# Kernel optimization log

Measured on AMD Instinct MI355X. Metric: run time of the kernel, lower is better.

The kernel has to match this reference:

```python
import jax, jax.numpy as jnp
import numpy as np

BIT = 8
QMAX = 2 ** (BIT - 1) - 1   # 127
QMIN = -(2 ** (BIT - 1))    # -128


def _quant_linear(x, W, b, act_sf):
    """HAWQ-style QuantLinear: per-output-channel symmetric 8-bit weights,
    integer GEMM on the (already-quantized) activation grid, dequantized output.
    Returns (out, weight_scaling_factor)."""
    w_sf = jnp.max(jnp.abs(W), axis=1) / QMAX                      # [out]
    w_int = jnp.clip(jnp.round(W / w_sf[:, None]), QMIN, QMAX)     # [out,in]
    x_int = x / act_sf                                             # integer-valued floats
    b_int = jnp.round(b / (w_sf * act_sf))                         # [out]
    out = (jnp.einsum('bsd,od->bso', x_int, w_int) + b_int) * (w_sf * act_sf)
    return out, w_sf


def _quant_act(x):
    """QuantAct: per-tensor symmetric 8-bit requantization."""
    sf = jnp.max(jnp.abs(x)) / QMAX
    xq = jnp.clip(jnp.round(x / sf), QMIN, QMAX) * sf
    return xq, sf


def setup_inputs() -> dict:
    key = jax.random.key(0)
    k = jax.random.split(key, 5)
    B, S, D, H = 256, 196, 384, 1536
    act_scaling_factor = jnp.array([0.05], jnp.float32)
    x = jax.random.normal(k[0], (B, S, D), jnp.float32)
    # input arrives already fake-quantized on the act_scaling_factor grid
    x = jnp.clip(jnp.round(x / act_scaling_factor), QMIN, QMAX) * act_scaling_factor
    W1 = jax.random.normal(k[1], (H, D), jnp.float32) * 0.02
    b1 = jax.random.normal(k[2], (H,), jnp.float32) * 0.02
    W2 = jax.random.normal(k[3], (D, H), jnp.float32) * 0.02
    b2 = jax.random.normal(k[4], (D,), jnp.float32) * 0.02
    return dict(x=x, W1=W1, b1=b1, W2=W2, b2=b2,
                act_scaling_factor=act_scaling_factor)


def reference(x, W1, b1, W2, b2, act_scaling_factor):
    h, _ = _quant_linear(x, W1, b1, act_scaling_factor)
    h = jax.nn.relu(h)
    h, asf1 = _quant_act(h)
    y, _ = _quant_linear(h, W2, b2, asf1)
    y, asf2 = _quant_act(y)
    return y, asf2
```

## Files before the change

kernel.cpp:

```cpp
#include <hip/hip_runtime.h>
#include <hip/hip_bf16.h>
#include <stdint.h>


#define M_TOT 50176
#define D_IN  384
#define H_MID 1536
#define OUT_N (M_TOT * D_IN)
#define NSLOT 256

typedef int v4i __attribute__((ext_vector_type(4)));

__device__ __forceinline__ float clamp_q(float q) {
  return fminf(fmaxf(q, -128.0f), 127.0f);
}

__device__ __forceinline__ float fast_div(float t, float d, float R) {
  const float q1 = t * R;
  const float r  = fmaf(-d, q1, t);
  return fmaf(r, R, q1);
}

__device__ __forceinline__ void gld_lds16(const int8_t* g, int8_t* s) {
  __builtin_amdgcn_global_load_lds((const __attribute__((address_space(1))) void*)g,
                                   (__attribute__((address_space(3))) void*)s,
                                   16, 0, 0);
}


__global__ void quant_w_kernel(const float* __restrict__ W, const float* __restrict__ b,
                               int8_t* __restrict__ Wq, float* __restrict__ wsf,
                               int* __restrict__ bint, const float* __restrict__ asf_p,
                               int cols) {
  const int lane = threadIdx.x & 63;
  const int row  = blockIdx.x * 4 + (threadIdx.x >> 6);
  const float* wr = W + (size_t)row * cols;
  float m = 0.f;
  for (int c = lane; c < cols; c += 64) m = fmaxf(m, fabsf(wr[c]));
#pragma unroll
  for (int off = 32; off; off >>= 1) m = fmaxf(m, __shfl_xor(m, off));
  const float sf = m / 127.0f;
  int8_t* qbase = Wq + (size_t)(row >> 4) * 16 * cols + (row & 15) * 16;
  for (int c = lane; c < cols; c += 64)
    qbase[(c >> 4) * 256 + (c & 15)] = (int8_t)clamp_q(rintf(wr[c] / sf));
  if (lane == 0) {
    wsf[row] = sf;
    if (bint) bint[row] = (int)rintf(b[row] / (sf * asf_p[0]));
  }
}

__global__ void quant_x_kernel(const float* __restrict__ x, int8_t* __restrict__ xq,
                               const float* __restrict__ asf_p) {
  const int lane = threadIdx.x & 63;
  const int wid  = threadIdx.x >> 6;
  const float R = 1.0f / asf_p[0];
  const int r  = lane & 15;
  const int kq = lane >> 4;
  const int ntask = (M_TOT / 16) * 6;
  for (int task = blockIdx.x * 4 + wid; task < ntask; task += gridDim.x * 4) {
    const int pan = task / 6;
    const int kcq = task - pan * 6;
    const float* src = x + ((size_t)pan * 16 + r) * D_IN + (kcq * 4 + kq) * 16;
    int out[4];
#pragma unroll
    for (int q4 = 0; q4 < 4; ++q4) {
      float4 v = *(const float4*)(src + q4 * 4);
      unsigned a0 = (unsigned char)(signed char)clamp_q(rintf(v.x * R));
      unsigned a1 = (unsigned char)(signed char)clamp_q(rintf(v.y * R));
      unsigned a2 = (unsigned char)(signed char)clamp_q(rintf(v.z * R));
      unsigned a3 = (unsigned char)(signed char)clamp_q(rintf(v.w * R));
      out[q4] = (int)(a0 | (a1 << 8) | (a2 << 16) | (a3 << 24));
    }
    *(int4*)(xq + (size_t)pan * 6144 + kcq * 1024 + lane * 16) = *(int4*)out;
  }
}

template <int MODE>
__global__ __launch_bounds__(512, 4) void gemm1_i8_kernel(
    const int8_t* __restrict__ A, const int8_t* __restrict__ Bm,
    const float* __restrict__ sfv, const int* __restrict__ bintv,
    const float* __restrict__ asf_p, const unsigned* __restrict__ gmax_in,
    int8_t* __restrict__ Cq, unsigned* __restrict__ gmax_out) {
  const int K = D_IN;
  __shared__ __align__(16) int8_t sA[2][8192];
  __shared__ __align__(16) int8_t sB[2][16384];
  const int tid    = threadIdx.x;
  const int lane   = tid & 63;
  const int wid    = tid >> 6;
  const int wr     = wid >> 2;
  const int wc     = wid & 3;
  const int tid16  = tid * 16;
  const int lane16 = lane * 16;
  const int l16    = lane & 15;
  const int r0     = (lane >> 4) * 4;
  const int cpx = gridDim.x >> 3;
  const int wg  = (blockIdx.x & 7) * cpx + (blockIdx.x >> 3);
  const int bm = wg % (H_MID / 128);
  const int bn = wg / (H_MID / 128);

  const int8_t* gA0 = A  + (size_t)(bm * 8)  * (16 * K);
  const int8_t* gB0 = Bm + (size_t)(bn * 16) * (16 * K);
  const int fA = tid16;
  const int baseA = (fA >> 10) * 16 * K + (fA & 1023);
  int baseB[2];
#pragma unroll
  for (int l = 0; l < 2; ++l) {
    const int f = l * 8192 + tid16;
    baseB[l] = (f >> 10) * 16 * K + (f & 1023);
  }

  v4i acc[4][4] = {};
  const int niter = K >> 6;

  gld_lds16(gA0 + baseA, &sA[0][tid16]);
#pragma unroll
  for (int l = 0; l < 2; ++l) gld_lds16(gB0 + baseB[l], &sB[0][l * 8192 + tid16]);

  for (int c = 0; c < niter; ++c) {
    const int buf = c & 1;
    if (c + 1 < niter) {
      const int co = (c + 1) << 10;
      gld_lds16(gA0 + baseA + co, &sA[buf ^ 1][tid16]);
#pragma unroll
      for (int l = 0; l < 2; ++l)
        gld_lds16(gB0 + baseB[l] + co, &sB[buf ^ 1][l * 8192 + tid16]);
      asm volatile("s_waitcnt vmcnt(3)" ::: "memory");
    } else {
      asm volatile("s_waitcnt vmcnt(0)" ::: "memory");
    }
    __builtin_amdgcn_s_barrier();
    __builtin_amdgcn_sched_barrier(0);
    v4i af[4], bf[4];
#pragma unroll
    for (int i = 0; i < 4; ++i)
      af[i] = *(const v4i*)&sA[buf][(wr * 4 + i) * 1024 + lane16];
#pragma unroll
    for (int j = 0; j < 4; ++j)
      bf[j] = *(const v4i*)&sB[buf][(wc * 4 + j) * 1024 + lane16];
#pragma unroll
    for (int i = 0; i < 4; ++i)
#pragma unroll
      for (int j = 0; j < 4; ++j)
        acc[i][j] = __builtin_amdgcn_mfma_i32_16x16x64_i8(af[i], bf[j], acc[i][j], 0, 0, 0);
    __builtin_amdgcn_sched_barrier(0);
    __builtin_amdgcn_s_barrier();
  }

  float lmax = 0.f;
  if (MODE == 0) {
    const float asf = asf_p[0];
#pragma unroll
    for (int i = 0; i < 4; ++i) {
      const int hbase = bm * 128 + wr * 64 + i * 16 + r0;
#pragma unroll
      for (int r = 0; r < 4; ++r) {
        int mi = acc[i][0][r];
#pragma unroll
        for (int j = 1; j < 4; ++j) mi = max(mi, acc[i][j][r]);
        const int h = hbase + r;
        lmax = fmaxf(lmax, (float)(mi + bintv[h]) * (sfv[h] * asf));
      }
    }
#pragma unroll
    for (int off = 32; off; off >>= 1) lmax = fmaxf(lmax, __shfl_xor(lmax, off));
    if (lane == 0) atomicMax(&gmax_out[(wg * 8 + wid) & (NSLOT - 1)], __float_as_uint(lmax));
  } else {
    float m = fmaxf(fmaxf(__uint_as_float(gmax_in[lane]),
                          __uint_as_float(gmax_in[lane + 64])),
                    fmaxf(__uint_as_float(gmax_in[lane + 128]),
                          __uint_as_float(gmax_in[lane + 192])));
#pragma unroll
    for (int off = 32; off; off >>= 1) m = fmaxf(m, __shfl_xor(m, off));
    const float sf1 = m / 127.0f;
    const float asf = asf_p[0];
    const float R   = 1.0f / sf1;
#pragma unroll
    for (int i = 0; i < 4; ++i) {
      const int hbase = bm * 128 + wr * 64 + i * 16 + r0;
      const int htile = bm * 8 + wr * 4 + i;
      float ratio[4];
      int bi4[4];
#pragma unroll
      for (int r = 0; r < 4; ++r) {
        const int h = hbase + r;
        ratio[r] = fast_div(sfv[h] * asf, sf1, R);
        bi4[r]   = bintv[h];
      }
#pragma unroll
      for (int j = 0; j < 4; ++j) {
        const int mm = bn * 256 + wc * 64 + j * 16 + l16;
        unsigned d = 0;
#pragma unroll
        for (int r = 0; r < 4; ++r) {
          const float f = (float)(acc[i][j][r] + bi4[r]);
          const int q = (int)fminf(fmaxf(rintf(f * ratio[r]), 0.f), 127.f);
          d |= (unsigned)q << (8 * r);
        }
        *(unsigned*)(Cq + (size_t)(mm >> 4) * 24576 + htile * 256 + (mm & 15) * 16 + r0) = d;
      }
    }
  }
}

__global__ __launch_bounds__(256, 4) void gemm2_i8_kernel(
    const int8_t* __restrict__ A, const int8_t* __restrict__ Bm,
    const float* __restrict__ sfv, const float* __restrict__ bias,
    const unsigned* __restrict__ gmax_in,
    float* __restrict__ Cout, unsigned* __restrict__ gmax_out) {
  const int K = H_MID;
  __shared__ __align__(16) int8_t sA[2][8192];
  __shared__ __align__(16) int8_t sB[2][8192];
  const int tid    = threadIdx.x;
  const int lane   = tid & 63;
  const int wid    = tid >> 6;
  const int wr     = wid >> 1;
  const int wc     = wid & 1;
  const int tid16  = tid * 16;
  const int lane16 = lane * 16;
  const int l16    = lane & 15;
  const int r0     = (lane >> 4) * 4;
  const int cpx = gridDim.x >> 3;
  const int wg  = (blockIdx.x & 7) * cpx + (blockIdx.x >> 3);
  const int bm = wg / (D_IN / 128);
  const int bn = wg % (D_IN / 128);

  const int8_t* gA0 = A  + (size_t)(bm * 8) * (16 * K);
  const int8_t* gB0 = Bm + (size_t)(bn * 8) * (16 * K);
  int base[2];
#pragma unroll
  for (int l = 0; l < 2; ++l) {
    const int f = l * 4096 + tid16;
    base[l] = (f >> 10) * 16 * K + (f & 1023);
  }

  v4i acc[4][4] = {};
  const int niter = K >> 6;

#pragma unroll
  for (int l = 0; l < 2; ++l) gld_lds16(gA0 + base[l], &sA[0][l * 4096 + tid16]);
#pragma unroll
  for (int l = 0; l < 2; ++l) gld_lds16(gB0 + base[l], &sB[0][l * 4096 + tid16]);

  for (int c = 0; c < niter; ++c) {
    const int buf = c & 1;
    if (c + 1 < niter) {
      const int co = (c + 1) << 10;
#pragma unroll
      for (int l = 0; l < 2; ++l)
        gld_lds16(gA0 + base[l] + co, &sA[buf ^ 1][l * 4096 + tid16]);
#pragma unroll
      for (int l = 0; l < 2; ++l)
        gld_lds16(gB0 + base[l] + co, &sB[buf ^ 1][l * 4096 + tid16]);
      asm volatile("s_waitcnt vmcnt(4)" ::: "memory");
    } else {
      asm volatile("s_waitcnt vmcnt(0)" ::: "memory");
    }
    __builtin_amdgcn_s_barrier();
    __builtin_amdgcn_sched_barrier(0);
    v4i af[4], bf[4];
#pragma unroll
    for (int i = 0; i < 4; ++i)
      af[i] = *(const v4i*)&sA[buf][(wr * 4 + i) * 1024 + lane16];
#pragma unroll
    for (int j = 0; j < 4; ++j)
      bf[j] = *(const v4i*)&sB[buf][(wc * 4 + j) * 1024 + lane16];
#pragma unroll
    for (int i = 0; i < 4; ++i)
#pragma unroll
      for (int j = 0; j < 4; ++j)
        acc[i][j] = __builtin_amdgcn_mfma_i32_16x16x64_i8(af[i], bf[j], acc[i][j], 0, 0, 0);
    __builtin_amdgcn_sched_barrier(0);
    __builtin_amdgcn_s_barrier();
  }

  float m = fmaxf(fmaxf(__uint_as_float(gmax_in[lane]),
                        __uint_as_float(gmax_in[lane + 64])),
                  fmaxf(__uint_as_float(gmax_in[lane + 128]),
                        __uint_as_float(gmax_in[lane + 192])));
#pragma unroll
  for (int off = 32; off; off >>= 1) m = fmaxf(m, __shfl_xor(m, off));
  const float sf1 = m / 127.0f;

  float lmax = 0.f;
#pragma unroll
  for (int j = 0; j < 4; ++j) {
    const int d = bn * 128 + wc * 64 + j * 16 + l16;
    const float scale = sfv[d] * sf1;
    const int bi = (int)rintf(bias[d] / scale);
    int mi = acc[0][j][0], mn = acc[0][j][0];
#pragma unroll
    for (int i = 0; i < 4; ++i) {
      const int row = bm * 128 + wr * 64 + i * 16 + r0;
#pragma unroll
      for (int r = 0; r < 4; ++r) {
        const int a = acc[i][j][r];
        mi = max(mi, a); mn = min(mn, a);
        Cout[(size_t)(row + r) * D_IN + d] = (float)(a + bi) * scale;
      }
    }
    lmax = fmaxf(lmax, fmaxf(fabsf((float)(mi + bi) * scale),
                             fabsf((float)(mn + bi) * scale)));
  }
#pragma unroll
  for (int off = 32; off; off >>= 1) lmax = fmaxf(lmax, __shfl_xor(lmax, off));
  if (lane == 0) atomicMax(&gmax_out[(wg * 4 + wid) & (NSLOT - 1)], __float_as_uint(lmax));
}

__global__ void final_quant_kernel(float* __restrict__ y, const unsigned* __restrict__ slots,
                                   int n4) {
  __shared__ float s_sf;
  const int tid = threadIdx.x;
  if (tid < 64) {
    float m = fmaxf(fmaxf(__uint_as_float(slots[tid]),
                          __uint_as_float(slots[tid + 64])),
                    fmaxf(__uint_as_float(slots[tid + 128]),
                          __uint_as_float(slots[tid + 192])));
#pragma unroll
    for (int off = 32; off; off >>= 1) m = fmaxf(m, __shfl_xor(m, off));
    if (tid == 0) s_sf = m / 127.0f;
  }
  __syncthreads();
  const float asf2 = s_sf;
  const float R = 1.0f / asf2;
  float4* y4 = (float4*)y;
  const int stride = gridDim.x * blockDim.x;
  for (int i = blockIdx.x * blockDim.x + tid; i < n4; i += stride) {
    float4 v = y4[i];
    v.x = clamp_q(rintf(fast_div(v.x, asf2, R))) * asf2;
    v.y = clamp_q(rintf(fast_div(v.y, asf2, R))) * asf2;
    v.z = clamp_q(rintf(fast_div(v.z, asf2, R))) * asf2;
    v.w = clamp_q(rintf(fast_div(v.w, asf2, R))) * asf2;
    y4[i] = v;
  }
  if (blockIdx.x == 0 && tid == 0) y[(size_t)n4 * 4] = asf2;
}

extern "C" void kernel_launch(void* const* d_in, const int* in_sizes, int n_in,
                              void* d_out, int out_size, void* d_ws, size_t ws_size,
                              hipStream_t stream) {
  const float* x   = (const float*)d_in[0];
  const float* W1  = (const float*)d_in[1];
  const float* b1  = (const float*)d_in[2];
  const float* W2  = (const float*)d_in[3];
  const float* b2  = (const float*)d_in[4];
  const float* asf = (const float*)d_in[5];

  char* ws = (char*)d_ws;
  unsigned* gmax1 = (unsigned*)ws;
  unsigned* gmax2 = (unsigned*)(ws + 1024);
  size_t off = 4096;
  int8_t* xq   = (int8_t*)(ws + off); off += (size_t)M_TOT * D_IN;
  int8_t* w1q  = (int8_t*)(ws + off); off += (size_t)H_MID * D_IN;
  float*  w1sf = (float*)(ws + off);  off += (size_t)H_MID * 4;
  int*    b1i  = (int*)(ws + off);    off += (size_t)H_MID * 4;
  int8_t* w2q  = (int8_t*)(ws + off); off += (size_t)D_IN * H_MID;
  float*  w2sf = (float*)(ws + off);  off += (size_t)D_IN * 4;
  off = (off + 255) & ~(size_t)255;
  int8_t* hq   = (int8_t*)(ws + off); off += (size_t)M_TOT * H_MID;

  hipMemsetAsync(d_ws, 0, 4096, stream);

  quant_w_kernel<<<H_MID / 4, 256, 0, stream>>>(W1, b1, w1q, w1sf, b1i, asf, D_IN);
  quant_w_kernel<<<D_IN / 4, 256, 0, stream>>>(W2, nullptr, w2q, w2sf, nullptr, nullptr, H_MID);
  quant_x_kernel<<<2048, 256, 0, stream>>>(x, xq, asf);

  const int g1 = (H_MID / 128) * (M_TOT / 256);
  const int g2 = (M_TOT / 128) * (D_IN / 128);
  gemm1_i8_kernel<0><<<g1, 512, 0, stream>>>(
      w1q, xq, w1sf, b1i, asf, nullptr, nullptr, gmax1);
  gemm1_i8_kernel<1><<<g1, 512, 0, stream>>>(
      w1q, xq, w1sf, b1i, asf, gmax1, hq, nullptr);
  gemm2_i8_kernel<<<g2, 256, 0, stream>>>(
      hq, w2q, w2sf, b2, gmax1, (float*)d_out, gmax2);
  final_quant_kernel<<<2048, 256, 0, stream>>>((float*)d_out, gmax2, OUT_N / 4);
}
```

Baseline: 196.6 us.

## Load weight fragments directly into registers, stage only activations in LDS

Both int8 GEMMs now read the weight operand straight from global memory into per-wave register double buffers instead of staging it through LDS, so only the activation tile uses shared memory. GEMM1 shrinks from 512-thread 128x256 tiles to 256-thread 128x128 tiles, doubling its grid, and the K loop is unrolled by two to alternate the register buffers. This is meant to cut LDS traffic and footprint and raise occupancy. In exchange, waves that share a weight panel each load it separately from global memory, and the smaller GEMM1 tiles reuse each weight load across fewer activation rows.

Result: slower. 228.0 us (+16.0%).

```diff
diff --git a/kernel.cpp b/kernel.cpp
--- a/kernel.cpp
+++ b/kernel.cpp
@@ -76,19 +76,18 @@
 }
 
 template <int MODE>
-__global__ __launch_bounds__(512, 4) void gemm1_i8_kernel(
-    const int8_t* __restrict__ A, const int8_t* __restrict__ Bm,
+__global__ __launch_bounds__(256, 4) void gemm1_i8_kernel(
+    const int8_t* __restrict__ Wq, const int8_t* __restrict__ Xq,
     const float* __restrict__ sfv, const int* __restrict__ bintv,
     const float* __restrict__ asf_p, const unsigned* __restrict__ gmax_in,
     int8_t* __restrict__ Cq, unsigned* __restrict__ gmax_out) {
   const int K = D_IN;
-  __shared__ __align__(16) int8_t sA[2][8192];
-  __shared__ __align__(16) int8_t sB[2][16384];
+  __shared__ __align__(16) int8_t sV[2][8192];
   const int tid    = threadIdx.x;
   const int lane   = tid & 63;
   const int wid    = tid >> 6;
-  const int wr     = wid >> 2;
-  const int wc     = wid & 3;
+  const int wr     = wid >> 1;
+  const int wc     = wid & 1;
   const int tid16  = tid * 16;
   const int lane16 = lane * 16;
   const int l16    = lane & 15;
@@ -98,53 +97,59 @@
   const int bm = wg % (H_MID / 128);
   const int bn = wg / (H_MID / 128);
 
-  const int8_t* gA0 = A  + (size_t)(bm * 8)  * (16 * K);
-  const int8_t* gB0 = Bm + (size_t)(bn * 16) * (16 * K);
-  const int fA = tid16;
-  const int baseA = (fA >> 10) * 16 * K + (fA & 1023);
-  int baseB[2];
+  const int sK = 16 * K;
+  const int8_t* pa = Wq + (size_t)(bm * 8 + wr * 4) * sK + lane16;
+  const int8_t* gV = Xq + (size_t)(bn * 8) * sK;
+  int baseV[2];
 #pragma unroll
   for (int l = 0; l < 2; ++l) {
-    const int f = l * 8192 + tid16;
-    baseB[l] = (f >> 10) * 16 * K + (f & 1023);
+    const int f = l * 4096 + tid16;
+    baseV[l] = (f >> 10) * sK + (f & 1023);
   }
 
   v4i acc[4][4] = {};
+  v4i d0[4], d1[4];
   const int niter = K >> 6;
 
-  gld_lds16(gA0 + baseA, &sA[0][tid16]);
-#pragma unroll
-  for (int l = 0; l < 2; ++l) gld_lds16(gB0 + baseB[l], &sB[0][l * 8192 + tid16]);
-
-  for (int c = 0; c < niter; ++c) {
-    const int buf = c & 1;
-    if (c + 1 < niter) {
-      const int co = (c + 1) << 10;
-      gld_lds16(gA0 + baseA + co, &sA[buf ^ 1][tid16]);
-#pragma unroll
-      for (int l = 0; l < 2; ++l)
-        gld_lds16(gB0 + baseB[l] + co, &sB[buf ^ 1][l * 8192 + tid16]);
-      asm volatile("s_waitcnt vmcnt(3)" ::: "memory");
-    } else {
-      asm volatile("s_waitcnt vmcnt(0)" ::: "memory");
-    }
-    __builtin_amdgcn_s_barrier();
-    __builtin_amdgcn_sched_barrier(0);
-    v4i af[4], bf[4];
-#pragma unroll
-    for (int i = 0; i < 4; ++i)
-      af[i] = *(const v4i*)&sA[buf][(wr * 4 + i) * 1024 + lane16];
-#pragma unroll
-    for (int j = 0; j < 4; ++j)
-      bf[j] = *(const v4i*)&sB[buf][(wc * 4 + j) * 1024 + lane16];
-#pragma unroll
-    for (int i = 0; i < 4; ++i)
-#pragma unroll
-      for (int j = 0; j < 4; ++j)
-        acc[i][j] = __builtin_amdgcn_mfma_i32_16x16x64_i8(af[i], bf[j], acc[i][j], 0, 0, 0);
-    __builtin_amdgcn_sched_barrier(0);
-    __builtin_amdgcn_s_barrier();
-  }
+#pragma unroll
+  for (int l = 0; l < 2; ++l) gld_lds16(gV + baseV[l], &sV[0][l * 4096 + tid16]);
+#pragma unroll
+  for (int i = 0; i < 4; ++i) d0[i] = *(const v4i*)(pa + i * sK);
+
+#define G1_BODY(c, buf, dc, dn)                                                   \
+  {                                                                               \
+    if ((c) + 1 < niter) {                                                        \
+      const int co = ((c) + 1) << 10;                                             \
+      _Pragma("unroll")                                                           \
+      for (int i = 0; i < 4; ++i) dn[i] = *(const v4i*)(pa + i * sK + co);        \
+      _Pragma("unroll")                                                           \
+      for (int l = 0; l < 2; ++l)                                                 \
+        gld_lds16(gV + baseV[l] + co, &sV[(buf) ^ 1][l * 4096 + tid16]);          \
+      asm volatile("s_waitcnt vmcnt(6)" ::: "memory");                            \
+    } else {                                                                      \
+      asm volatile("s_waitcnt vmcnt(0)" ::: "memory");                            \
+    }                                                                             \
+    __builtin_amdgcn_s_barrier();                                                 \
+    __builtin_amdgcn_sched_barrier(0);                                            \
+    v4i vf[4];                                                                    \
+    _Pragma("unroll")                                                             \
+    for (int j = 0; j < 4; ++j)                                                   \
+      vf[j] = *(const v4i*)&sV[(buf)][(wc * 4 + j) * 1024 + lane16];              \
+    _Pragma("unroll")                                                             \
+    for (int i = 0; i < 4; ++i)                                                   \
+      _Pragma("unroll")                                                           \
+      for (int j = 0; j < 4; ++j)                                                 \
+        acc[i][j] = __builtin_amdgcn_mfma_i32_16x16x64_i8(dc[i], vf[j],           \
+                                                          acc[i][j], 0, 0, 0);    \
+    __builtin_amdgcn_sched_barrier(0);                                            \
+    __builtin_amdgcn_s_barrier();                                                 \
+  }
+
+  for (int c = 0; c < niter; c += 2) {
+    G1_BODY(c,     0, d0, d1)
+    G1_BODY(c + 1, 1, d1, d0)
+  }
+#undef G1_BODY
 
   float lmax = 0.f;
   if (MODE == 0) {
@@ -163,7 +168,7 @@
     }
 #pragma unroll
     for (int off = 32; off; off >>= 1) lmax = fmaxf(lmax, __shfl_xor(lmax, off));
-    if (lane == 0) atomicMax(&gmax_out[(wg * 8 + wid) & (NSLOT - 1)], __float_as_uint(lmax));
+    if (lane == 0) atomicMax(&gmax_out[(wg * 4 + wid) & (NSLOT - 1)], __float_as_uint(lmax));
   } else {
     float m = fmaxf(fmaxf(__uint_as_float(gmax_in[lane]),
                           __uint_as_float(gmax_in[lane + 64])),
@@ -188,7 +193,7 @@
       }
 #pragma unroll
       for (int j = 0; j < 4; ++j) {
-        const int mm = bn * 256 + wc * 64 + j * 16 + l16;
+        const int mm = bn * 128 + wc * 64 + j * 16 + l16;
         unsigned d = 0;
 #pragma unroll
         for (int r = 0; r < 4; ++r) {
@@ -203,13 +208,12 @@
 }
 
 __global__ __launch_bounds__(256, 4) void gemm2_i8_kernel(
-    const int8_t* __restrict__ A, const int8_t* __restrict__ Bm,
+    const int8_t* __restrict__ Hq, const int8_t* __restrict__ W2q,
     const float* __restrict__ sfv, const float* __restrict__ bias,
     const unsigned* __restrict__ gmax_in,
     float* __restrict__ Cout, unsigned* __restrict__ gmax_out) {
   const int K = H_MID;
-  __shared__ __align__(16) int8_t sA[2][8192];
-  __shared__ __align__(16) int8_t sB[2][8192];
+  __shared__ __align__(16) int8_t sV[2][8192];
   const int tid    = threadIdx.x;
   const int lane   = tid & 63;
   const int wid    = tid >> 6;
@@ -224,54 +228,59 @@
   const int bm = wg / (D_IN / 128);
   const int bn = wg % (D_IN / 128);
 
-  const int8_t* gA0 = A  + (size_t)(bm * 8) * (16 * K);
-  const int8_t* gB0 = Bm + (size_t)(bn * 8) * (16 * K);
-  int base[2];
+  const int sK = 16 * K;
+  const int8_t* pb = W2q + (size_t)(bn * 8 + wc * 4) * sK + lane16;
+  const int8_t* gV = Hq + (size_t)(bm * 8) * sK;
+  int baseV[2];
 #pragma unroll
   for (int l = 0; l < 2; ++l) {
     const int f = l * 4096 + tid16;
-    base[l] = (f >> 10) * 16 * K + (f & 1023);
+    baseV[l] = (f >> 10) * sK + (f & 1023);
   }
 
   v4i acc[4][4] = {};
+  v4i d0[4], d1[4];
   const int niter = K >> 6;
 
 #pragma unroll
-  for (int l = 0; l < 2; ++l) gld_lds16(gA0 + base[l], &sA[0][l * 4096 + tid16]);
-#pragma unroll
-  for (int l = 0; l < 2; ++l) gld_lds16(gB0 + base[l], &sB[0][l * 4096 + tid16]);
-
-  for (int c = 0; c < niter; ++c) {
-    const int buf = c & 1;
-    if (c + 1 < niter) {
-      const int co = (c + 1) << 10;
-#pragma unroll
-      for (int l = 0; l < 2; ++l)
-        gld_lds16(gA0 + base[l] + co, &sA[buf ^ 1][l * 4096 + tid16]);
-#pragma unroll
-      for (int l = 0; l < 2; ++l)
-        gld_lds16(gB0 + base[l] + co, &sB[buf ^ 1][l * 4096 + tid16]);
-      asm volatile("s_waitcnt vmcnt(4)" ::: "memory");
-    } else {
-      asm volatile("s_waitcnt vmcnt(0)" ::: "memory");
-    }
-    __builtin_amdgcn_s_barrier();
-    __builtin_amdgcn_sched_barrier(0);
-    v4i af[4], bf[4];
-#pragma unroll
-    for (int i = 0; i < 4; ++i)
-      af[i] = *(const v4i*)&sA[buf][(wr * 4 + i) * 1024 + lane16];
-#pragma unroll
-    for (int j = 0; j < 4; ++j)
-      bf[j] = *(const v4i*)&sB[buf][(wc * 4 + j) * 1024 + lane16];
-#pragma unroll
-    for (int i = 0; i < 4; ++i)
-#pragma unroll
-      for (int j = 0; j < 4; ++j)
-        acc[i][j] = __builtin_amdgcn_mfma_i32_16x16x64_i8(af[i], bf[j], acc[i][j], 0, 0, 0);
-    __builtin_amdgcn_sched_barrier(0);
-    __builtin_amdgcn_s_barrier();
-  }
+  for (int l = 0; l < 2; ++l) gld_lds16(gV + baseV[l], &sV[0][l * 4096 + tid16]);
+#pragma unroll
+  for (int j = 0; j < 4; ++j) d0[j] = *(const v4i*)(pb + j * sK);
+
+#define G2_BODY(c, buf, dc, dn)                                                   \
+  {                                                                               \
+    if ((c) + 1 < niter) {                                                        \
+      const int co = ((c) + 1) << 10;                                             \
+      _Pragma("unroll")                                                           \
+      for (int j = 0; j < 4; ++j) dn[j] = *(const v4i*)(pb + j * sK + co);        \
+      _Pragma("unroll")                                                           \
+      for (int l = 0; l < 2; ++l)                                                 \
+        gld_lds16(gV + baseV[l] + co, &sV[(buf) ^ 1][l * 4096 + tid16]);          \
+      asm volatile("s_waitcnt vmcnt(6)" ::: "memory");                            \
+    } else {                                                                      \
+      asm volatile("s_waitcnt vmcnt(0)" ::: "memory");                            \
+    }                                                                             \
+    __builtin_amdgcn_s_barrier();                                                 \
+    __builtin_amdgcn_sched_barrier(0);                                            \
+    v4i af[4];                                                                    \
+    _Pragma("unroll")                                                             \
+    for (int i = 0; i < 4; ++i)                                                   \
+      af[i] = *(const v4i*)&sV[(buf)][(wr * 4 + i) * 1024 + lane16];              \
+    _Pragma("unroll")                                                             \
+    for (int i = 0; i < 4; ++i)                                                   \
+      _Pragma("unroll")                                                           \
+      for (int j = 0; j < 4; ++j)                                                 \
+        acc[i][j] = __builtin_amdgcn_mfma_i32_16x16x64_i8(af[i], dc[j],           \
+                                                          acc[i][j], 0, 0, 0);    \
+    __builtin_amdgcn_sched_barrier(0);                                            \
+    __builtin_amdgcn_s_barrier();                                                 \
+  }
+
+  for (int c = 0; c < niter; c += 2) {
+    G2_BODY(c,     0, d0, d1)
+    G2_BODY(c + 1, 1, d1, d0)
+  }
+#undef G2_BODY
 
   float m = fmaxf(fmaxf(__uint_as_float(gmax_in[lane]),
                         __uint_as_float(gmax_in[lane + 64])),
@@ -364,11 +373,11 @@
   quant_w_kernel<<<D_IN / 4, 256, 0, stream>>>(W2, nullptr, w2q, w2sf, nullptr, nullptr, H_MID);
   quant_x_kernel<<<2048, 256, 0, stream>>>(x, xq, asf);
 
-  const int g1 = (H_MID / 128) * (M_TOT / 256);
+  const int g1 = (H_MID / 128) * (M_TOT / 128);
   const int g2 = (M_TOT / 128) * (D_IN / 128);
-  gemm1_i8_kernel<0><<<g1, 512, 0, stream>>>(
+  gemm1_i8_kernel<0><<<g1, 256, 0, stream>>>(
       w1q, xq, w1sf, b1i, asf, nullptr, nullptr, gmax1);
-  gemm1_i8_kernel<1><<<g1, 512, 0, stream>>>(
+  gemm1_i8_kernel<1><<<g1, 256, 0, stream>>>(
       w1q, xq, w1sf, b1i, asf, gmax1, hq, nullptr);
   gemm2_i8_kernel<<<g2, 256, 0, stream>>>(
       hq, w2q, w2sf, b2, gmax1, (float*)d_out, gmax2);
```

## Switch int8 GEMMs to 32x32x32 MFMA with 32-row panel layout

Applied to the files above, without the earlier changes.

Replaces the 16x16x64 int8 MFMA tiles in both GEMM kernels with 32x32x32 MFMA instructions accumulating into 16-register outputs. The weight and activation quantization kernels now pack operands into 32-row panels so that each LDS fragment load feeds the larger instruction, and the epilogues are remapped to the 32x32 accumulator layout. The goal is fewer MFMA issues and fewer LDS fragment reads per unit of work, at the cost of a different output store pattern and reworked index math in every kernel.

After: 212.3 us. 8.0% more time.

```diff
diff --git a/kernel.cpp b/kernel.cpp
--- a/kernel.cpp
+++ b/kernel.cpp
@@ -9,7 +9,8 @@
 #define OUT_N (M_TOT * D_IN)
 #define NSLOT 256
 
-typedef int v4i __attribute__((ext_vector_type(4)));
+typedef int v4i  __attribute__((ext_vector_type(4)));
+typedef int v16i __attribute__((ext_vector_type(16)));
 
 __device__ __forceinline__ float clamp_q(float q) {
   return fminf(fmaxf(q, -128.0f), 127.0f);
@@ -26,7 +27,6 @@
                                    (__attribute__((address_space(3))) void*)s,
                                    16, 0, 0);
 }
-
 
 __global__ void quant_w_kernel(const float* __restrict__ W, const float* __restrict__ b,
                                int8_t* __restrict__ Wq, float* __restrict__ wsf,
@@ -40,9 +40,9 @@
 #pragma unroll
   for (int off = 32; off; off >>= 1) m = fmaxf(m, __shfl_xor(m, off));
   const float sf = m / 127.0f;
-  int8_t* qbase = Wq + (size_t)(row >> 4) * 16 * cols + (row & 15) * 16;
+  int8_t* qbase = Wq + (size_t)(row >> 5) * 32 * cols + (row & 31) * 16;
   for (int c = lane; c < cols; c += 64)
-    qbase[(c >> 4) * 256 + (c & 15)] = (int8_t)clamp_q(rintf(wr[c] / sf));
+    qbase[(c >> 4) * 512 + (c & 15)] = (int8_t)clamp_q(rintf(wr[c] / sf));
   if (lane == 0) {
     wsf[row] = sf;
     if (bint) bint[row] = (int)rintf(b[row] / (sf * asf_p[0]));
@@ -54,13 +54,13 @@
   const int lane = threadIdx.x & 63;
   const int wid  = threadIdx.x >> 6;
   const float R = 1.0f / asf_p[0];
-  const int r  = lane & 15;
-  const int kq = lane >> 4;
-  const int ntask = (M_TOT / 16) * 6;
+  const int r5 = lane & 31;
+  const int kh = lane >> 5;
+  const int ntask = (M_TOT / 32) * (D_IN / 32);
   for (int task = blockIdx.x * 4 + wid; task < ntask; task += gridDim.x * 4) {
-    const int pan = task / 6;
-    const int kcq = task - pan * 6;
-    const float* src = x + ((size_t)pan * 16 + r) * D_IN + (kcq * 4 + kq) * 16;
+    const int pan = task / 12;
+    const int t   = task - pan * 12;
+    const float* src = x + ((size_t)pan * 32 + r5) * D_IN + t * 32 + kh * 16;
     int out[4];
 #pragma unroll
     for (int q4 = 0; q4 < 4; ++q4) {
@@ -71,7 +71,7 @@
       unsigned a3 = (unsigned char)(signed char)clamp_q(rintf(v.w * R));
       out[q4] = (int)(a0 | (a1 << 8) | (a2 << 16) | (a3 << 24));
     }
-    *(int4*)(xq + (size_t)pan * 6144 + kcq * 1024 + lane * 16) = *(int4*)out;
+    *(int4*)(xq + (size_t)pan * (32 * D_IN) + t * 1024 + lane * 16) = *(int4*)out;
   }
 }
 
@@ -91,25 +91,24 @@
   const int wc     = wid & 3;
   const int tid16  = tid * 16;
   const int lane16 = lane * 16;
-  const int l16    = lane & 15;
-  const int r0     = (lane >> 4) * 4;
+  const int c5     = lane & 31;
+  const int hi     = lane >> 5;
   const int cpx = gridDim.x >> 3;
   const int wg  = (blockIdx.x & 7) * cpx + (blockIdx.x >> 3);
   const int bm = wg % (H_MID / 128);
   const int bn = wg / (H_MID / 128);
 
-  const int8_t* gA0 = A  + (size_t)(bm * 8)  * (16 * K);
-  const int8_t* gB0 = Bm + (size_t)(bn * 16) * (16 * K);
-  const int fA = tid16;
-  const int baseA = (fA >> 10) * 16 * K + (fA & 1023);
+  const int8_t* gA0 = A  + (size_t)(bm * 4) * (32 * K);
+  const int8_t* gB0 = Bm + (size_t)(bn * 8) * (32 * K);
+  const int baseA = (tid16 >> 11) * (32 * K) + (tid16 & 2047);
   int baseB[2];
 #pragma unroll
   for (int l = 0; l < 2; ++l) {
     const int f = l * 8192 + tid16;
-    baseB[l] = (f >> 10) * 16 * K + (f & 1023);
-  }
-
-  v4i acc[4][4] = {};
+    baseB[l] = (f >> 11) * (32 * K) + (f & 2047);
+  }
+
+  v16i acc[2][2] = {};
   const int niter = K >> 6;
 
   gld_lds16(gA0 + baseA, &sA[0][tid16]);
@@ -119,7 +118,7 @@
   for (int c = 0; c < niter; ++c) {
     const int buf = c & 1;
     if (c + 1 < niter) {
-      const int co = (c + 1) << 10;
+      const int co = (c + 1) << 11;
       gld_lds16(gA0 + baseA + co, &sA[buf ^ 1][tid16]);
 #pragma unroll
       for (int l = 0; l < 2; ++l)
@@ -130,18 +129,24 @@
     }
     __builtin_amdgcn_s_barrier();
     __builtin_amdgcn_sched_barrier(0);
-    v4i af[4], bf[4];
-#pragma unroll
-    for (int i = 0; i < 4; ++i)
-      af[i] = *(const v4i*)&sA[buf][(wr * 4 + i) * 1024 + lane16];
-#pragma unroll
-    for (int j = 0; j < 4; ++j)
-      bf[j] = *(const v4i*)&sB[buf][(wc * 4 + j) * 1024 + lane16];
-#pragma unroll
-    for (int i = 0; i < 4; ++i)
-#pragma unroll
-      for (int j = 0; j < 4; ++j)
-        acc[i][j] = __builtin_amdgcn_mfma_i32_16x16x64_i8(af[i], bf[j], acc[i][j], 0, 0, 0);
+    v4i af[2][2], bf[2][2];
+#pragma unroll
+    for (int ks = 0; ks < 2; ++ks) {
+#pragma unroll
+      for (int i = 0; i < 2; ++i)
+        af[ks][i] = *(const v4i*)&sA[buf][(wr * 2 + i) * 2048 + ks * 1024 + lane16];
+#pragma unroll
+      for (int j = 0; j < 2; ++j)
+        bf[ks][j] = *(const v4i*)&sB[buf][(wc * 2 + j) * 2048 + ks * 1024 + lane16];
+    }
+#pragma unroll
+    for (int ks = 0; ks < 2; ++ks)
+#pragma unroll
+      for (int i = 0; i < 2; ++i)
+#pragma unroll
+        for (int j = 0; j < 2; ++j)
+          acc[i][j] = __builtin_amdgcn_mfma_i32_32x32x32_i8(af[ks][i], bf[ks][j],
+                                                            acc[i][j], 0, 0, 0);
     __builtin_amdgcn_sched_barrier(0);
     __builtin_amdgcn_s_barrier();
   }
@@ -150,14 +155,12 @@
   if (MODE == 0) {
     const float asf = asf_p[0];
 #pragma unroll
-    for (int i = 0; i < 4; ++i) {
-      const int hbase = bm * 128 + wr * 64 + i * 16 + r0;
-#pragma unroll
-      for (int r = 0; r < 4; ++r) {
-        int mi = acc[i][0][r];
-#pragma unroll
-        for (int j = 1; j < 4; ++j) mi = max(mi, acc[i][j][r]);
-        const int h = hbase + r;
+    for (int i = 0; i < 2; ++i) {
+      const int hbase = bm * 128 + wr * 64 + i * 32;
+#pragma unroll
+      for (int reg = 0; reg < 16; ++reg) {
+        const int mi = max(acc[i][0][reg], acc[i][1][reg]);
+        const int h  = hbase + (reg & 3) + 8 * (reg >> 2) + 4 * hi;
         lmax = fmaxf(lmax, (float)(mi + bintv[h]) * (sfv[h] * asf));
       }
     }
@@ -175,35 +178,38 @@
     const float asf = asf_p[0];
     const float R   = 1.0f / sf1;
 #pragma unroll
-    for (int i = 0; i < 4; ++i) {
-      const int hbase = bm * 128 + wr * 64 + i * 16 + r0;
-      const int htile = bm * 8 + wr * 4 + i;
-      float ratio[4];
-      int bi4[4];
-#pragma unroll
-      for (int r = 0; r < 4; ++r) {
-        const int h = hbase + r;
-        ratio[r] = fast_div(sfv[h] * asf, sf1, R);
-        bi4[r]   = bintv[h];
+    for (int i = 0; i < 2; ++i) {
+#pragma unroll
+      for (int q = 0; q < 4; ++q) {
+        const int h0 = bm * 128 + wr * 64 + i * 32 + q * 8 + hi * 4;
+        float ratio[4];
+        int bi4[4];
+#pragma unroll
+        for (int r = 0; r < 4; ++r) {
+          const int h = h0 + r;
+          ratio[r] = fast_div(sfv[h] * asf, sf1, R);
+          bi4[r]   = bintv[h];
+        }
+#pragma unroll
+        for (int j = 0; j < 2; ++j) {
+          const int mm = bn * 256 + wc * 64 + j * 32 + c5;
+          unsigned d = 0;
+#pragma unroll
+          for (int r = 0; r < 4; ++r) {
+            const float f = (float)(acc[i][j][q * 4 + r] + bi4[r]);
+            const int qv = (int)fminf(fmaxf(rintf(f * ratio[r]), 0.f), 127.f);
+            d |= (unsigned)qv << (8 * r);
+          }
+          *(unsigned*)(Cq + (size_t)(mm >> 5) * 49152 + (h0 >> 4) * 512 +
+                       (mm & 31) * 16 + (h0 & 15)) = d;
+        }
       }
-#pragma unroll
-      for (int j = 0; j < 4; ++j) {
-        const int mm = bn * 256 + wc * 64 + j * 16 + l16;
-        unsigned d = 0;
-#pragma unroll
-        for (int r = 0; r < 4; ++r) {
-          const float f = (float)(acc[i][j][r] + bi4[r]);
-          const int q = (int)fminf(fmaxf(rintf(f * ratio[r]), 0.f), 127.f);
-          d |= (unsigned)q << (8 * r);
-        }
-        *(unsigned*)(Cq + (size_t)(mm >> 4) * 24576 + htile * 256 + (mm & 15) * 16 + r0) = d;
-      }
     }
   }
 }
 
 __global__ __launch_bounds__(256, 4) void gemm2_i8_kernel(
-    const int8_t* __restrict__ A, const int8_t* __restrict__ Bm,
+    const int8_t* __restrict__ Hq, const int8_t* __restrict__ W2q,
     const float* __restrict__ sfv, const float* __restrict__ bias,
     const unsigned* __restrict__ gmax_in,
     float* __restrict__ Cout, unsigned* __restrict__ gmax_out) {
@@ -217,23 +223,23 @@
   const int wc     = wid & 1;
   const int tid16  = tid * 16;
   const int lane16 = lane * 16;
-  const int l16    = lane & 15;
-  const int r0     = (lane >> 4) * 4;
+  const int c5     = lane & 31;
+  const int hi     = lane >> 5;
   const int cpx = gridDim.x >> 3;
   const int wg  = (blockIdx.x & 7) * cpx + (blockIdx.x >> 3);
   const int bm = wg / (D_IN / 128);
   const int bn = wg % (D_IN / 128);
 
-  const int8_t* gA0 = A  + (size_t)(bm * 8) * (16 * K);
-  const int8_t* gB0 = Bm + (size_t)(bn * 8) * (16 * K);
+  const int8_t* gA0 = Hq  + (size_t)(bm * 4) * (32 * K);
+  const int8_t* gB0 = W2q + (size_t)(bn * 4) * (32 * K);
   int base[2];
 #pragma unroll
   for (int l = 0; l < 2; ++l) {
     const int f = l * 4096 + tid16;
-    base[l] = (f >> 10) * 16 * K + (f & 1023);
-  }
-
-  v4i acc[4][4] = {};
+    base[l] = (f >> 11) * (32 * K) + (f & 2047);
+  }
+
+  v16i acc[2][2] = {};
   const int niter = K >> 6;
 
 #pragma unroll
@@ -244,7 +250,7 @@
   for (int c = 0; c < niter; ++c) {
     const int buf = c & 1;
     if (c + 1 < niter) {
-      const int co = (c + 1) << 10;
+      const int co = (c + 1) << 11;
 #pragma unroll
       for (int l = 0; l < 2; ++l)
         gld_lds16(gA0 + base[l] + co, &sA[buf ^ 1][l * 4096 + tid16]);
@@ -257,18 +263,24 @@
     }
     __builtin_amdgcn_s_barrier();
     __builtin_amdgcn_sched_barrier(0);
-    v4i af[4], bf[4];
-#pragma unroll
-    for (int i = 0; i < 4; ++i)
-      af[i] = *(const v4i*)&sA[buf][(wr * 4 + i) * 1024 + lane16];
-#pragma unroll
-    for (int j = 0; j < 4; ++j)
-      bf[j] = *(const v4i*)&sB[buf][(wc * 4 + j) * 1024 + lane16];
-#pragma unroll
-    for (int i = 0; i < 4; ++i)
-#pragma unroll
-      for (int j = 0; j < 4; ++j)
-        acc[i][j] = __builtin_amdgcn_mfma_i32_16x16x64_i8(af[i], bf[j], acc[i][j], 0, 0, 0);
+    v4i af[2][2], bf[2][2];
+#pragma unroll
+    for (int ks = 0; ks < 2; ++ks) {
+#pragma unroll
+      for (int i = 0; i < 2; ++i)
+        af[ks][i] = *(const v4i*)&sA[buf][(wr * 2 + i) * 2048 + ks * 1024 + lane16];
+#pragma unroll
+      for (int j = 0; j < 2; ++j)
+        bf[ks][j] = *(const v4i*)&sB[buf][(wc * 2 + j) * 2048 + ks * 1024 + lane16];
+    }
+#pragma unroll
+    for (int ks = 0; ks < 2; ++ks)
+#pragma unroll
+      for (int i = 0; i < 2; ++i)
+#pragma unroll
+        for (int j = 0; j < 2; ++j)
+          acc[i][j] = __builtin_amdgcn_mfma_i32_32x32x32_i8(af[ks][i], bf[ks][j],
+                                                            acc[i][j], 0, 0, 0);
     __builtin_amdgcn_sched_barrier(0);
     __builtin_amdgcn_s_barrier();
   }
@@ -283,19 +295,20 @@
 
   float lmax = 0.f;
 #pragma unroll
-  for (int j = 0; j < 4; ++j) {
-    const int d = bn * 128 + wc * 64 + j * 16 + l16;
+  for (int j = 0; j < 2; ++j) {
+    const int d = bn * 128 + wc * 64 + j * 32 + c5;
     const float scale = sfv[d] * sf1;
     const int bi = (int)rintf(bias[d] / scale);
     int mi = acc[0][j][0], mn = acc[0][j][0];
 #pragma unroll
-    for (int i = 0; i < 4; ++i) {
-      const int row = bm * 128 + wr * 64 + i * 16 + r0;
-#pragma unroll
-      for (int r = 0; r < 4; ++r) {
-        const int a = acc[i][j][r];
+    for (int i = 0; i < 2; ++i) {
+      const int rbase = bm * 128 + wr * 64 + i * 32;
+#pragma unroll
+      for (int reg = 0; reg < 16; ++reg) {
+        const int a = acc[i][j][reg];
         mi = max(mi, a); mn = min(mn, a);
-        Cout[(size_t)(row + r) * D_IN + d] = (float)(a + bi) * scale;
+        const int row = rbase + (reg & 3) + 8 * (reg >> 2) + 4 * hi;
+        Cout[(size_t)row * D_IN + d] = (float)(a + bi) * scale;
       }
     }
     lmax = fmaxf(lmax, fmaxf(fabsf((float)(mi + bi) * scale),
```
